# Kernel tuning notes

Hardware: AMD Instinct MI355X
Metric: run time of the kernel (lower is better)

## Reference

```python
import jax, jax.numpy as jnp
import numpy as np
from jax import lax

# --- static config (mirrors Kernel.__init__ defaults + chosen production scale) ---
B, IN_CH, OUT_CH = 8, 1, 6
H = W = 64
KS, STRIDE, PAD = 5, 1, 0
DEV, NIN, NCTRL = 5, 5, 2            # 5 devices x (5 input + 2 control) = 7 electrodes
HOUT = (H + 2 * PAD - KS) // STRIDE + 1   # 60
L = HOUT * HOUT                       # unfold window count
# inputs_list = [1,2,3,4,5] per device -> control_list = np.delete(range(7), inputs) = [0,6]
# torch.gather(data, -1, cat(inputs, controls)) with data = cat(x_vals, ctrl_vals):
IDX = jnp.array([1, 2, 3, 4, 5, 0, 6])
WIDTHS = [7, 90, 90, 90, 1]


def setup_inputs() -> dict:
    key = jax.random.key(0)
    ks = jax.random.split(key, 2 + 2 * (len(WIDTHS) - 1))
    inp = {
        'x': jax.random.normal(ks[0], (B, IN_CH, H, W), jnp.float32),
        'all_controls': jax.random.uniform(ks[1], (OUT_CH, IN_CH, DEV, NCTRL), jnp.float32),
    }
    for i in range(len(WIDTHS) - 1):
        inp[f'W{i}'] = jax.random.normal(ks[2 + 2 * i], (WIDTHS[i], WIDTHS[i + 1]), jnp.float32) * 0.1
        inp[f'b{i}'] = jax.random.normal(ks[3 + 2 * i], (WIDTHS[i + 1],), jnp.float32) * 0.1
    return inp


def _forward(x, all_controls, Ws, bs):
    # F.unfold: conv_general_dilated_patches yields channels ordered (c, kh, kw),
    # identical to torch unfold's C*K*K channel layout.
    patches = lax.conv_general_dilated_patches(
        x, (KS, KS), (STRIDE, STRIDE), 'VALID')           # [B, C*K*K, HOUT, WOUT]
    patches = patches.reshape(B, IN_CH, KS * KS, L)        # [B, C, 25, L]
    # transpose(3,4) then split 25 -> (device_no, n_inputs)
    xw = jnp.transpose(patches, (0, 1, 3, 2)).reshape(B, IN_CH, L, DEV, NIN)
    # repeat_interleave over out_channels -> pure broadcast
    xw = jnp.broadcast_to(xw[:, None], (B, OUT_CH, IN_CH, L, DEV, NIN))
    ctrl = jnp.broadcast_to(all_controls[None, :, :, None],
                            (B, OUT_CH, IN_CH, L, DEV, NCTRL))
    # cat(inputs, controls) then gather into electrode order (amplitude is None -> no affine map)
    data = jnp.concatenate([xw, ctrl], axis=-1)[..., IDX]  # [B, out, C, L, DEV, 7]
    h = data.reshape(-1, WIDTHS[0])                        # flatten for the processor MLP
    for Wm, bm in zip(Ws[:-1], bs[:-1]):
        h = jax.nn.relu(h @ Wm + bm)
    h = h @ Ws[-1] + bs[-1]                                # [N, 1]
    res = h.reshape(B, OUT_CH, IN_CH, L, DEV).sum(axis=4).sum(axis=2)  # [B, out, L]
    # F.fold with kernel_size=1 is just a reshape of L -> (HOUT, HOUT)
    return res.reshape(B, OUT_CH, HOUT, HOUT)


def reference(x, all_controls, W0, b0, W1, b1, W2, b2, W3, b3):
    return _forward(x, all_controls, [W0, W1, W2, W3], [b0, b1, b2, b3])
```

## Files before the change

kernel.cpp:

```cpp
#include <hip/hip_runtime.h>

typedef unsigned short u16;
typedef unsigned int u32;
typedef __attribute__((ext_vector_type(8))) short short8;
typedef __attribute__((ext_vector_type(4))) float f32x4;

#define WS_W3T  0
#define WS_W0F  384
#define WS_W1F  37248
#define WS_W2F  55680

__device__ __forceinline__ u16 f2b(float f) {
  union { u32 i; float f; } v; v.f = f;
  u32 i = v.i;
  return (u16)((i + 0x7FFFu + ((i >> 16) & 1u)) >> 16);
}

__device__ __forceinline__ u32 cvtpk(float lo, float hi) {
  u32 r;
  asm("v_cvt_pk_bf16_f32 %0, %1, %2" : "=v"(r) : "v"(lo), "v"(hi));
  return r;
}

__device__ __forceinline__ void lds_compiler_fence() {
  asm volatile("" ::: "memory");
}

__global__ void prep_kernel(const float* __restrict__ ac, const float* __restrict__ W0,
                            const float* __restrict__ b0, const float* __restrict__ W1,
                            const float* __restrict__ b1, const float* __restrict__ W2,
                            const float* __restrict__ b2, const float* __restrict__ W3,
                            const float* __restrict__ b3,
                            float* __restrict__ w3t, u16* __restrict__ W0f,
                            u16* __restrict__ W1f, u16* __restrict__ W2f) {
  int tid = blockIdx.x * blockDim.x + threadIdx.x;
  int nth = gridDim.x * blockDim.x;
  for (int i = tid; i < 96; i += nth)
    w3t[i] = (i < 90) ? W3[i] : ((i == 90) ? b3[0] : 0.0f);
  for (int i = tid; i < 6 * 6 * 64 * 8; i += nth) {
    int o = i / 3072, rem = i % 3072;
    int t = rem >> 9, lane = (rem >> 3) & 63, jj = rem & 7;
    int q = lane >> 4, m = lane & 15;
    int k = q * 8 + jj;
    int u = t * 16 + m;
    u16 v = 0;
    if (k < 5) {
      const int rowmap[5] = {5, 0, 1, 2, 3};
      if (u < 90) v = f2b(W0[rowmap[k] * 90 + u]);
    } else if (k < 10) {
      int dd = k - 5;
      if (u < 90) {
        float c0 = ac[(o * 5 + dd) * 2 + 0], c1 = ac[(o * 5 + dd) * 2 + 1];
        v = f2b(b0[u] + c0 * W0[4 * 90 + u] + c1 * W0[6 * 90 + u]);
      } else if (u == 90) {
        v = (u16)0x3F80;
      }
    }
    W0f[i] = v;
  }
  for (int i = tid; i < 2 * 18 * 64 * 8; i += nth) {
    int which = i / (18 * 64 * 8);
    int j2 = i % (18 * 64 * 8);
    int jj = j2 & 7, lane = (j2 >> 3) & 63, f = j2 >> 9;
    int t = f / 3, ki = f % 3;
    int qA = lane >> 4, m = lane & 15;
    int row = 32 * ki + 16 * (jj >> 2) + 4 * qA + (jj & 3);
    int col = 16 * t + m;
    const float* W = which ? W2 : W1;
    const float* bb = which ? b2 : b1;
    u16 v = 0;
    if (row < 90 && col < 90) v = f2b(W[row * 90 + col]);
    else if (row == 90) v = (col < 90) ? f2b(bb[col]) : ((col == 90) ? (u16)0x3F80 : (u16)0);
    (which ? W2f : W1f)[j2] = v;
  }
}

__device__ __forceinline__ f32x4 mfma16(short8 a, short8 b, f32x4 c) {
  return __builtin_amdgcn_mfma_f32_16x16x32_bf16(a, b, c, 0, 0, 0);
}

__device__ __forceinline__ short8 packB(const f32x4& a0, const f32x4& a1) {
  union { u32 u[4]; short8 s; } fu;
  fu.u[0] = cvtpk(fmaxf(a0.x, 0.f), fmaxf(a0.y, 0.f));
  fu.u[1] = cvtpk(fmaxf(a0.z, 0.f), fmaxf(a0.w, 0.f));
  fu.u[2] = cvtpk(fmaxf(a1.x, 0.f), fmaxf(a1.y, 0.f));
  fu.u[3] = cvtpk(fmaxf(a1.z, 0.f), fmaxf(a1.w, 0.f));
  return fu.s;
}

#define ISS(D0, D1, D2, BASE, OFF)                                   \
  do {                                                               \
    D0 = (BASE)[(OFF)];                                              \
    D1 = (BASE)[(OFF) + 64];                                         \
    D2 = (BASE)[(OFF) + 128];                                        \
    lds_compiler_fence();                                            \
  } while (0)

#define MM3(F0, F1, F2, IA0, IA1, IA2, IB0, IB1, IB2, VA, VB)        \
  do {                                                               \
    VA = mfma16(F0, IA0, z4); VB = mfma16(F0, IB0, z4);              \
    VA = mfma16(F1, IA1, VA); VB = mfma16(F1, IB1, VB);              \
    VA = mfma16(F2, IA2, VA); VB = mfma16(F2, IB2, VB);              \
  } while (0)

#define DOT4(V, WV, ACC)                                             \
  ACC += fmaxf((V).x, 0.f) * (WV).x + fmaxf((V).y, 0.f) * (WV).y +   \
         fmaxf((V).z, 0.f) * (WV).z + fmaxf((V).w, 0.f) * (WV).w

__global__ __launch_bounds__(512, 2) void mlp_kernel(
    const float* __restrict__ x, const float* __restrict__ w3t,
    const u16* __restrict__ W0f, const u16* __restrict__ W1f,
    const u16* __restrict__ W2f, float* __restrict__ out) {
  __shared__ short8 ldsW1[18 * 64];
  __shared__ short8 ldsW2[18 * 64];
  const int tid = threadIdx.x;
  {
    const uint4* s1 = (const uint4*)W1f;
    const uint4* s2 = (const uint4*)W2f;
    uint4* d1 = (uint4*)ldsW1;
    uint4* d2 = (uint4*)ldsW2;
#pragma unroll
    for (int i = 0; i < 3; ++i) {
      int j = tid + i * 512;
      if (j < 1152) { d1[j] = s1[j]; d2[j] = s2[j]; }
    }
  }
  __syncthreads();

  const int lane = tid & 63;
  const int wv = tid >> 6;
  const int q = lane >> 4, n = lane & 15;

  const int g = blockIdx.x * 8 + wv;
  const int o = g % 6;
  const int f = g / 6;

  short8 w0f[6];
  const short8* p0 = (const short8*)W0f + o * 384;
#pragma unroll
  for (int t = 0; t < 6; ++t) w0f[t] = p0[t * 64 + lane];
  f32x4 w3v[6];
#pragma unroll
  for (int t = 0; t < 6; ++t) w3v[t] = *(const f32x4*)(w3t + t * 16 + q * 4);

  const int bb = f / 225, idx = f % 225;
  const int seg0 = bb * 6 + o;
  const int l0 = idx * 16;
  const int l = l0 + n;
  const int oh = l / 60, ow = l - oh * 60;
  const float* xrow0 = x + (bb * 4096 + oh * 64 + ow);
  const float* xrow1 = xrow0 + 4 * 4096;

  const short8* w1base = &ldsW1[0] + lane;
  const short8* w2base = &ldsW2[0] + lane;

  const f32x4 z4 = {0.f, 0.f, 0.f, 0.f};
  float outAcc0 = 0.f, outAcc1 = 0.f;

  float pa0 = xrow0[0], pa1 = xrow0[1], pa2 = xrow0[2], pa3 = xrow0[3], pa4 = xrow0[4];
  float pb0 = xrow1[0], pb1 = xrow1[1], pb2 = xrow1[2], pb3 = xrow1[3], pb4 = xrow1[4];

#pragma unroll 1
  for (int d = 0; d < 5; ++d) {
    float a0 = pa0, a1 = pa1, a2 = pa2, a3 = pa3, a4 = pa4;
    float b0 = pb0, b1 = pb1, b2 = pb2, b3 = pb3, b4 = pb4;
    if (d < 4) {
      const float* xp0 = xrow0 + (d + 1) * 64;
      const float* xp1 = xrow1 + (d + 1) * 64;
      pa0 = xp0[0]; pa1 = xp0[1]; pa2 = xp0[2]; pa3 = xp0[3]; pa4 = xp0[4];
      pb0 = xp1[0]; pb1 = xp1[1]; pb2 = xp1[2]; pb3 = xp1[3]; pb4 = xp1[4];
    }

    const u32 u3c = (d == 1) ? 0x00003F80u : ((d == 2) ? 0x3F800000u : 0u);
    const u32 q1c = (d == 3) ? 0x00003F80u : ((d == 4) ? 0x3F800000u : 0u);
    const float k5f = (d == 0) ? 1.0f : 0.0f;

    union { u32 u[4]; short8 s; } bu0, bu1;
    u32 ta = cvtpk(a0, a1), tb = cvtpk(b0, b1);
    bu0.u[0] = (q == 1) ? q1c : ta;
    bu1.u[0] = (q == 1) ? q1c : tb;
    bu0.u[1] = cvtpk(a2, a3);  bu1.u[1] = cvtpk(b2, b3);
    bu0.u[2] = cvtpk(a4, k5f); bu1.u[2] = cvtpk(b4, k5f);
    bu0.u[3] = u3c;            bu1.u[3] = u3c;
    short8 bx0 = bu0.s, bx1 = bu1.s;

    short8 A0, A1, A2, B0, B1, B2;
    ISS(A0, A1, A2, w1base, 0);

    short8 h00, h01, h02, h10, h11, h12;
    {
      f32x4 t0 = mfma16(w0f[0], bx0, z4);
      f32x4 t1 = mfma16(w0f[1], bx0, z4);
      f32x4 t2 = mfma16(w0f[0], bx1, z4);
      f32x4 t3 = mfma16(w0f[1], bx1, z4);
      h00 = packB(t0, t1); h10 = packB(t2, t3);
      t0 = mfma16(w0f[2], bx0, z4); t1 = mfma16(w0f[3], bx0, z4);
      t2 = mfma16(w0f[2], bx1, z4); t3 = mfma16(w0f[3], bx1, z4);
      h01 = packB(t0, t1); h11 = packB(t2, t3);
      t0 = mfma16(w0f[4], bx0, z4); t1 = mfma16(w0f[5], bx0, z4);
      t2 = mfma16(w0f[4], bx1, z4); t3 = mfma16(w0f[5], bx1, z4);
      h02 = packB(t0, t1); h12 = packB(t2, t3);
    }

    short8 g00, g01, g02, g10, g11, g12;
    f32x4 vX0, vX1, vY0, vY1;

    ISS(B0, B1, B2, w1base, 192);
    MM3(A0, A1, A2, h00, h01, h02, h10, h11, h12, vX0, vX1);
    ISS(A0, A1, A2, w1base, 384);
    MM3(B0, B1, B2, h00, h01, h02, h10, h11, h12, vY0, vY1);
    g00 = packB(vX0, vY0); g10 = packB(vX1, vY1);
    ISS(B0, B1, B2, w1base, 384 + 192);
    MM3(A0, A1, A2, h00, h01, h02, h10, h11, h12, vX0, vX1);
    ISS(A0, A1, A2, w1base, 768);
    MM3(B0, B1, B2, h00, h01, h02, h10, h11, h12, vY0, vY1);
    g01 = packB(vX0, vY0); g11 = packB(vX1, vY1);
    ISS(B0, B1, B2, w1base, 768 + 192);
    MM3(A0, A1, A2, h00, h01, h02, h10, h11, h12, vX0, vX1);
    ISS(A0, A1, A2, w2base, 0);
    MM3(B0, B1, B2, h00, h01, h02, h10, h11, h12, vY0, vY1);
    g02 = packB(vX0, vY0); g12 = packB(vX1, vY1);

    ISS(B0, B1, B2, w2base, 192);
    MM3(A0, A1, A2, g00, g01, g02, g10, g11, g12, vX0, vX1);
    ISS(A0, A1, A2, w2base, 384);
    MM3(B0, B1, B2, g00, g01, g02, g10, g11, g12, vY0, vY1);
    DOT4(vX0, w3v[0], outAcc0); DOT4(vY0, w3v[1], outAcc0);
    DOT4(vX1, w3v[0], outAcc1); DOT4(vY1, w3v[1], outAcc1);
    ISS(B0, B1, B2, w2base, 384 + 192);
    MM3(A0, A1, A2, g00, g01, g02, g10, g11, g12, vX0, vX1);
    ISS(A0, A1, A2, w2base, 768);
    MM3(B0, B1, B2, g00, g01, g02, g10, g11, g12, vY0, vY1);
    DOT4(vX0, w3v[2], outAcc0); DOT4(vY0, w3v[3], outAcc0);
    DOT4(vX1, w3v[2], outAcc1); DOT4(vY1, w3v[3], outAcc1);
    ISS(B0, B1, B2, w2base, 768 + 192);
    MM3(A0, A1, A2, g00, g01, g02, g10, g11, g12, vX0, vX1);
    MM3(B0, B1, B2, g00, g01, g02, g10, g11, g12, vY0, vY1);
    DOT4(vX0, w3v[4], outAcc0); DOT4(vY0, w3v[5], outAcc0);
    DOT4(vX1, w3v[4], outAcc1); DOT4(vY1, w3v[5], outAcc1);
  }

  outAcc0 += __shfl_xor(outAcc0, 16, 64);
  outAcc0 += __shfl_xor(outAcc0, 32, 64);
  outAcc1 += __shfl_xor(outAcc1, 16, 64);
  outAcc1 += __shfl_xor(outAcc1, 32, 64);
  if (lane < 16) {
    out[seg0 * 3600 + l0 + lane] = outAcc0;
    out[(seg0 + 24) * 3600 + l0 + lane] = outAcc1;
  }
}

extern "C" void kernel_launch(void* const* d_in, const int* in_sizes, int n_in,
                              void* d_out, int out_size, void* d_ws, size_t ws_size,
                              hipStream_t stream) {
  const float* x  = (const float*)d_in[0];
  const float* ac = (const float*)d_in[1];
  const float* W0 = (const float*)d_in[2];
  const float* b0 = (const float*)d_in[3];
  const float* W1 = (const float*)d_in[4];
  const float* b1 = (const float*)d_in[5];
  const float* W2 = (const float*)d_in[6];
  const float* b2 = (const float*)d_in[7];
  const float* W3 = (const float*)d_in[8];
  const float* b3 = (const float*)d_in[9];
  float* out = (float*)d_out;
  char* ws = (char*)d_ws;
  float* w3t = (float*)(ws + WS_W3T);
  u16* W0f = (u16*)(ws + WS_W0F);
  u16* W1f = (u16*)(ws + WS_W1F);
  u16* W2f = (u16*)(ws + WS_W2F);
  prep_kernel<<<128, 256, 0, stream>>>(ac, W0, b0, W1, b1, W2, b2, W3, b3,
                                       w3t, W0f, W1f, W2f);
  mlp_kernel<<<675, 512, 0, stream>>>(x, w3t, W0f, W1f, W2f, out);
}
```

Before: 110.8 us.

## Triple-buffer LDS weight fragments across loop iterations and raise MFMA priority

Moves from two to three register buffers for the W1/W2 LDS fragments. Loads are issued two stages ahead, and the first fragments for the next device iteration are prefetched at the end of the current one, so the layer-0 MFMAs no longer wait on LDS reads. MFMA blocks are also wrapped in s_setprio(1)/s_setprio(0) so they are favoured when waves are interleaved. The extra short8 registers raise VGPR pressure, which could hurt the occupancy of 2 blocks of 512 threads.

```diff
diff --git a/kernel.cpp b/kernel.cpp
--- a/kernel.cpp
+++ b/kernel.cpp
@@ -98,9 +98,11 @@
 
 #define MM3(F0, F1, F2, IA0, IA1, IA2, IB0, IB1, IB2, VA, VB)        \
   do {                                                               \
+    __builtin_amdgcn_s_setprio(1);                                   \
     VA = mfma16(F0, IA0, z4); VB = mfma16(F0, IB0, z4);              \
     VA = mfma16(F1, IA1, VA); VB = mfma16(F1, IB1, VB);              \
     VA = mfma16(F2, IA2, VA); VB = mfma16(F2, IB2, VB);              \
+    __builtin_amdgcn_s_setprio(0);                                   \
   } while (0)
 
 #define DOT4(V, WV, ACC)                                             \
@@ -160,6 +162,10 @@
   float pa0 = xrow0[0], pa1 = xrow0[1], pa2 = xrow0[2], pa3 = xrow0[3], pa4 = xrow0[4];
   float pb0 = xrow1[0], pb1 = xrow1[1], pb2 = xrow1[2], pb3 = xrow1[3], pb4 = xrow1[4];
 
+  short8 A0, A1, A2, B0, B1, B2, C0, C1, C2;
+  ISS(A0, A1, A2, w1base, 0);
+  ISS(B0, B1, B2, w1base, 192);
+
 #pragma unroll 1
   for (int d = 0; d < 5; ++d) {
     float a0 = pa0, a1 = pa1, a2 = pa2, a3 = pa3, a4 = pa4;
@@ -184,58 +190,62 @@
     bu0.u[3] = u3c;            bu1.u[3] = u3c;
     short8 bx0 = bu0.s, bx1 = bu1.s;
 
-    short8 A0, A1, A2, B0, B1, B2;
-    ISS(A0, A1, A2, w1base, 0);
-
     short8 h00, h01, h02, h10, h11, h12;
     {
+      __builtin_amdgcn_s_setprio(1);
       f32x4 t0 = mfma16(w0f[0], bx0, z4);
       f32x4 t1 = mfma16(w0f[1], bx0, z4);
       f32x4 t2 = mfma16(w0f[0], bx1, z4);
       f32x4 t3 = mfma16(w0f[1], bx1, z4);
+      __builtin_amdgcn_s_setprio(0);
       h00 = packB(t0, t1); h10 = packB(t2, t3);
+      __builtin_amdgcn_s_setprio(1);
       t0 = mfma16(w0f[2], bx0, z4); t1 = mfma16(w0f[3], bx0, z4);
       t2 = mfma16(w0f[2], bx1, z4); t3 = mfma16(w0f[3], bx1, z4);
+      __builtin_amdgcn_s_setprio(0);
       h01 = packB(t0, t1); h11 = packB(t2, t3);
+      __builtin_amdgcn_s_setprio(1);
       t0 = mfma16(w0f[4], bx0, z4); t1 = mfma16(w0f[5], bx0, z4);
       t2 = mfma16(w0f[4], bx1, z4); t3 = mfma16(w0f[5], bx1, z4);
+      __builtin_amdgcn_s_setprio(0);
       h02 = packB(t0, t1); h12 = packB(t2, t3);
     }
 
     short8 g00, g01, g02, g10, g11, g12;
     f32x4 vX0, vX1, vY0, vY1;
 
-    ISS(B0, B1, B2, w1base, 192);
+    ISS(C0, C1, C2, w1base, 384);
     MM3(A0, A1, A2, h00, h01, h02, h10, h11, h12, vX0, vX1);
-    ISS(A0, A1, A2, w1base, 384);
+    ISS(A0, A1, A2, w1base, 576);
     MM3(B0, B1, B2, h00, h01, h02, h10, h11, h12, vY0, vY1);
     g00 = packB(vX0, vY0); g10 = packB(vX1, vY1);
-    ISS(B0, B1, B2, w1base, 384 + 192);
-    MM3(A0, A1, A2, h00, h01, h02, h10, h11, h12, vX0, vX1);
-    ISS(A0, A1, A2, w1base, 768);
-    MM3(B0, B1, B2, h00, h01, h02, h10, h11, h12, vY0, vY1);
+    ISS(B0, B1, B2, w1base, 768);
+    MM3(C0, C1, C2, h00, h01, h02, h10, h11, h12, vX0, vX1);
+    ISS(C0, C1, C2, w1base, 960);
+    MM3(A0, A1, A2, h00, h01, h02, h10, h11, h12, vY0, vY1);
     g01 = packB(vX0, vY0); g11 = packB(vX1, vY1);
-    ISS(B0, B1, B2, w1base, 768 + 192);
-    MM3(A0, A1, A2, h00, h01, h02, h10, h11, h12, vX0, vX1);
     ISS(A0, A1, A2, w2base, 0);
-    MM3(B0, B1, B2, h00, h01, h02, h10, h11, h12, vY0, vY1);
+    MM3(B0, B1, B2, h00, h01, h02, h10, h11, h12, vX0, vX1);
+    ISS(B0, B1, B2, w2base, 192);
+    MM3(C0, C1, C2, h00, h01, h02, h10, h11, h12, vY0, vY1);
     g02 = packB(vX0, vY0); g12 = packB(vX1, vY1);
 
-    ISS(B0, B1, B2, w2base, 192);
+    ISS(C0, C1, C2, w2base, 384);
     MM3(A0, A1, A2, g00, g01, g02, g10, g11, g12, vX0, vX1);
-    ISS(A0, A1, A2, w2base, 384);
+    ISS(A0, A1, A2, w2base, 576);
     MM3(B0, B1, B2, g00, g01, g02, g10, g11, g12, vY0, vY1);
     DOT4(vX0, w3v[0], outAcc0); DOT4(vY0, w3v[1], outAcc0);
     DOT4(vX1, w3v[0], outAcc1); DOT4(vY1, w3v[1], outAcc1);
-    ISS(B0, B1, B2, w2base, 384 + 192);
-    MM3(A0, A1, A2, g00, g01, g02, g10, g11, g12, vX0, vX1);
-    ISS(A0, A1, A2, w2base, 768);
-    MM3(B0, B1, B2, g00, g01, g02, g10, g11, g12, vY0, vY1);
+    ISS(B0, B1, B2, w2base, 768);
+    MM3(C0, C1, C2, g00, g01, g02, g10, g11, g12, vX0, vX1);
+    ISS(C0, C1, C2, w2base, 960);
+    MM3(A0, A1, A2, g00, g01, g02, g10, g11, g12, vY0, vY1);
     DOT4(vX0, w3v[2], outAcc0); DOT4(vY0, w3v[3], outAcc0);
     DOT4(vX1, w3v[2], outAcc1); DOT4(vY1, w3v[3], outAcc1);
-    ISS(B0, B1, B2, w2base, 768 + 192);
-    MM3(A0, A1, A2, g00, g01, g02, g10, g11, g12, vX0, vX1);
-    MM3(B0, B1, B2, g00, g01, g02, g10, g11, g12, vY0, vY1);
+    ISS(A0, A1, A2, w1base, 0);
+    MM3(B0, B1, B2, g00, g01, g02, g10, g11, g12, vX0, vX1);
+    ISS(B0, B1, B2, w1base, 192);
+    MM3(C0, C1, C2, g00, g01, g02, g10, g11, g12, vY0, vY1);
     DOT4(vX0, w3v[4], outAcc0); DOT4(vY0, w3v[5], outAcc0);
     DOT4(vX1, w3v[4], outAcc1); DOT4(vY1, w3v[5], outAcc1);
   }
```

New measurement: 119.2 us. +7.6%, slower.

## Fuse weight preparation into the MLP kernel and drop the prep launch

Applied to the files above, without the earlier changes.

Removes the separate prep kernel that converted and swizzled the weights into a workspace. Each block of the MLP kernel now builds the bf16 W1/W2 fragments directly in LDS from the fp32 weights, and each wave builds its own W0 fragment (with the controls folded in) and its W3 vector in registers. This removes one kernel launch and the serialization between the two kernels. In exchange every one of the 675 blocks repeats the conversion work and reads scattered fp32 weights, which adds per-block startup latency.

```diff
diff --git a/kernel.cpp b/kernel.cpp
--- a/kernel.cpp
+++ b/kernel.cpp
@@ -5,11 +5,6 @@
 typedef __attribute__((ext_vector_type(8))) short short8;
 typedef __attribute__((ext_vector_type(4))) float f32x4;
 
-#define WS_W3T  0
-#define WS_W0F  384
-#define WS_W1F  37248
-#define WS_W2F  55680
-
 __device__ __forceinline__ u16 f2b(float f) {
   union { u32 i; float f; } v; v.f = f;
   u32 i = v.i;
@@ -24,55 +19,6 @@
 
 __device__ __forceinline__ void lds_compiler_fence() {
   asm volatile("" ::: "memory");
-}
-
-__global__ void prep_kernel(const float* __restrict__ ac, const float* __restrict__ W0,
-                            const float* __restrict__ b0, const float* __restrict__ W1,
-                            const float* __restrict__ b1, const float* __restrict__ W2,
-                            const float* __restrict__ b2, const float* __restrict__ W3,
-                            const float* __restrict__ b3,
-                            float* __restrict__ w3t, u16* __restrict__ W0f,
-                            u16* __restrict__ W1f, u16* __restrict__ W2f) {
-  int tid = blockIdx.x * blockDim.x + threadIdx.x;
-  int nth = gridDim.x * blockDim.x;
-  for (int i = tid; i < 96; i += nth)
-    w3t[i] = (i < 90) ? W3[i] : ((i == 90) ? b3[0] : 0.0f);
-  for (int i = tid; i < 6 * 6 * 64 * 8; i += nth) {
-    int o = i / 3072, rem = i % 3072;
-    int t = rem >> 9, lane = (rem >> 3) & 63, jj = rem & 7;
-    int q = lane >> 4, m = lane & 15;
-    int k = q * 8 + jj;
-    int u = t * 16 + m;
-    u16 v = 0;
-    if (k < 5) {
-      const int rowmap[5] = {5, 0, 1, 2, 3};
-      if (u < 90) v = f2b(W0[rowmap[k] * 90 + u]);
-    } else if (k < 10) {
-      int dd = k - 5;
-      if (u < 90) {
-        float c0 = ac[(o * 5 + dd) * 2 + 0], c1 = ac[(o * 5 + dd) * 2 + 1];
-        v = f2b(b0[u] + c0 * W0[4 * 90 + u] + c1 * W0[6 * 90 + u]);
-      } else if (u == 90) {
-        v = (u16)0x3F80;
-      }
-    }
-    W0f[i] = v;
-  }
-  for (int i = tid; i < 2 * 18 * 64 * 8; i += nth) {
-    int which = i / (18 * 64 * 8);
-    int j2 = i % (18 * 64 * 8);
-    int jj = j2 & 7, lane = (j2 >> 3) & 63, f = j2 >> 9;
-    int t = f / 3, ki = f % 3;
-    int qA = lane >> 4, m = lane & 15;
-    int row = 32 * ki + 16 * (jj >> 2) + 4 * qA + (jj & 3);
-    int col = 16 * t + m;
-    const float* W = which ? W2 : W1;
-    const float* bb = which ? b2 : b1;
-    u16 v = 0;
-    if (row < 90 && col < 90) v = f2b(W[row * 90 + col]);
-    else if (row == 90) v = (col < 90) ? f2b(bb[col]) : ((col == 90) ? (u16)0x3F80 : (u16)0);
-    (which ? W2f : W1f)[j2] = v;
-  }
 }
 
 __device__ __forceinline__ f32x4 mfma16(short8 a, short8 b, f32x4 c) {
@@ -108,25 +54,15 @@
          fmaxf((V).z, 0.f) * (WV).z + fmaxf((V).w, 0.f) * (WV).w
 
 __global__ __launch_bounds__(512, 2) void mlp_kernel(
-    const float* __restrict__ x, const float* __restrict__ w3t,
-    const u16* __restrict__ W0f, const u16* __restrict__ W1f,
-    const u16* __restrict__ W2f, float* __restrict__ out) {
+    const float* __restrict__ x, const float* __restrict__ ac,
+    const float* __restrict__ W0, const float* __restrict__ b0,
+    const float* __restrict__ W1, const float* __restrict__ b1,
+    const float* __restrict__ W2, const float* __restrict__ b2,
+    const float* __restrict__ W3, const float* __restrict__ b3,
+    float* __restrict__ out) {
   __shared__ short8 ldsW1[18 * 64];
   __shared__ short8 ldsW2[18 * 64];
   const int tid = threadIdx.x;
-  {
-    const uint4* s1 = (const uint4*)W1f;
-    const uint4* s2 = (const uint4*)W2f;
-    uint4* d1 = (uint4*)ldsW1;
-    uint4* d2 = (uint4*)ldsW2;
-#pragma unroll
-    for (int i = 0; i < 3; ++i) {
-      int j = tid + i * 512;
-      if (j < 1152) { d1[j] = s1[j]; d2[j] = s2[j]; }
-    }
-  }
-  __syncthreads();
-
   const int lane = tid & 63;
   const int wv = tid >> 6;
   const int q = lane >> 4, n = lane & 15;
@@ -135,13 +71,71 @@
   const int o = g % 6;
   const int f = g / 6;
 
+  {
+    u16* lds1u = (u16*)ldsW1;
+    u16* lds2u = (u16*)ldsW2;
+    for (int i2 = tid; i2 < 2 * 9216; i2 += 512) {
+      const int which = i2 / 9216;
+      const int rc = i2 - which * 9216;
+      const int row = rc / 96, col = rc - row * 96;
+      const float* W = which ? W2 : W1;
+      const float* bb = which ? b2 : b1;
+      u16 v = 0;
+      if (row < 90 && col < 90) v = f2b(W[row * 90 + col]);
+      else if (row == 90) v = (col < 90) ? f2b(bb[col]) : ((col == 90) ? (u16)0x3F80 : (u16)0);
+      const int t = col >> 4, m = col & 15;
+      const int ki = row >> 5, r5 = row & 31;
+      const int jj = ((r5 >> 4) << 2) | (r5 & 3);
+      const int qA = (r5 >> 2) & 3;
+      const int ln = (qA << 4) | m;
+      const int j2 = (((t * 3 + ki) << 9) | (ln << 3)) | jj;
+      (which ? lds2u : lds1u)[j2] = v;
+    }
+  }
+
   short8 w0f[6];
-  const short8* p0 = (const short8*)W0f + o * 384;
-#pragma unroll
-  for (int t = 0; t < 6; ++t) w0f[t] = p0[t * 64 + lane];
+  {
+    const int m = lane & 15;
+    const int k0 = q * 8;
+#pragma unroll
+    for (int t = 0; t < 6; ++t) {
+      const int u = t * 16 + m;
+      union { u16 e[8]; short8 s; } fr;
+#pragma unroll
+      for (int jj = 0; jj < 8; ++jj) {
+        const int k = k0 + jj;
+        u16 v = 0;
+        if (k < 5) {
+          const int rm = (k == 0) ? 5 : (k - 1);
+          if (u < 90) v = f2b(W0[rm * 90 + u]);
+        } else if (k < 10) {
+          const int dd = k - 5;
+          if (u < 90) {
+            float c0 = ac[(o * 5 + dd) * 2 + 0], c1 = ac[(o * 5 + dd) * 2 + 1];
+            v = f2b(b0[u] + c0 * W0[4 * 90 + u] + c1 * W0[6 * 90 + u]);
+          } else if (u == 90) {
+            v = (u16)0x3F80;
+          }
+        }
+        fr.e[jj] = v;
+      }
+      w0f[t] = fr.s;
+    }
+  }
+
   f32x4 w3v[6];
 #pragma unroll
-  for (int t = 0; t < 6; ++t) w3v[t] = *(const f32x4*)(w3t + t * 16 + q * 4);
+  for (int t = 0; t < 6; ++t) {
+    f32x4 wvv;
+#pragma unroll
+    for (int j = 0; j < 4; ++j) {
+      const int u = t * 16 + q * 4 + j;
+      wvv[j] = (u < 90) ? W3[u] : ((u == 90) ? b3[0] : 0.0f);
+    }
+    w3v[t] = wvv;
+  }
+
+  __syncthreads();
 
   const int bb = f / 225, idx = f % 225;
   const int seg0 = bb * 6 + o;
@@ -163,7 +157,7 @@
 #pragma unroll 1
   for (int d = 0; d < 5; ++d) {
     float a0 = pa0, a1 = pa1, a2 = pa2, a3 = pa3, a4 = pa4;
-    float b0 = pb0, b1 = pb1, b2 = pb2, b3 = pb3, b4 = pb4;
+    float b0v = pb0, b1v = pb1, b2v = pb2, b3v = pb3, b4v = pb4;
     if (d < 4) {
       const float* xp0 = xrow0 + (d + 1) * 64;
       const float* xp1 = xrow1 + (d + 1) * 64;
@@ -176,12 +170,12 @@
     const float k5f = (d == 0) ? 1.0f : 0.0f;
 
     union { u32 u[4]; short8 s; } bu0, bu1;
-    u32 ta = cvtpk(a0, a1), tb = cvtpk(b0, b1);
+    u32 ta = cvtpk(a0, a1), tb = cvtpk(b0v, b1v);
     bu0.u[0] = (q == 1) ? q1c : ta;
     bu1.u[0] = (q == 1) ? q1c : tb;
-    bu0.u[1] = cvtpk(a2, a3);  bu1.u[1] = cvtpk(b2, b3);
-    bu0.u[2] = cvtpk(a4, k5f); bu1.u[2] = cvtpk(b4, k5f);
-    bu0.u[3] = u3c;            bu1.u[3] = u3c;
+    bu0.u[1] = cvtpk(a2, a3);   bu1.u[1] = cvtpk(b2v, b3v);
+    bu0.u[2] = cvtpk(a4, k5f);  bu1.u[2] = cvtpk(b4v, k5f);
+    bu0.u[3] = u3c;             bu1.u[3] = u3c;
     short8 bx0 = bu0.s, bx1 = bu1.s;
 
     short8 A0, A1, A2, B0, B1, B2;
@@ -264,12 +258,6 @@
   const float* W3 = (const float*)d_in[8];
   const float* b3 = (const float*)d_in[9];
   float* out = (float*)d_out;
-  char* ws = (char*)d_ws;
-  float* w3t = (float*)(ws + WS_W3T);
-  u16* W0f = (u16*)(ws + WS_W0F);
-  u16* W1f = (u16*)(ws + WS_W1F);
-  u16* W2f = (u16*)(ws + WS_W2F);
-  prep_kernel<<<128, 256, 0, stream>>>(ac, W0, b0, W1, b1, W2, b2, W3, b3,
-                                       w3t, W0f, W1f, W2f);
-  mlp_kernel<<<675, 512, 0, stream>>>(x, w3t, W0f, W1f, W2f, out);
-}
+  (void)d_ws; (void)ws_size;
+  mlp_kernel<<<675, 512, 0, stream>>>(x, ac, W0, b0, W1, b1, W2, b2, W3, b3, out);
+}
```

Result: slower. 166.5 us (+50.3%).
